# Kernel tuning notes

Measured on AMD Instinct MI355X. Metric: run time of the kernel, lower is better.

Reference implementation:

```python
import jax, jax.numpy as jnp
import numpy as np

C = 256
GROUPS = 8
EPS_GN = 1e-5
EPS_ATTN = 1e-6


def setup_inputs() -> dict:
    key = jax.random.key(0)
    ks = jax.random.split(key, 10)
    b, c, h, w = 8, C, 128, 128
    # xavier_uniform for 1x1 conv weight [out, in]: limit = sqrt(6/(in+out))
    lim = float(np.sqrt(6.0 / (c + c)))
    mkw = lambda k: jax.random.uniform(k, (c, c), jnp.float32, -lim, lim)
    return {
        "x": jax.random.normal(ks[0], (b, c, h, w), jnp.float32),
        "gamma": jnp.ones((c,), jnp.float32),
        "beta": jnp.zeros((c,), jnp.float32),
        "Wq": mkw(ks[1]), "bq": jnp.zeros((c,), jnp.float32),
        "Wk": mkw(ks[2]), "bk": jnp.zeros((c,), jnp.float32),
        "Wv": mkw(ks[3]), "bv": jnp.zeros((c,), jnp.float32),
        "Wp": mkw(ks[4]), "bp": jnp.zeros((c,), jnp.float32),
    }


def _group_norm(x, gamma, beta):
    b, c, h, w = x.shape
    xg = x.reshape(b, GROUPS, c // GROUPS, h, w)
    mean = xg.mean(axis=(2, 3, 4), keepdims=True)
    var = xg.var(axis=(2, 3, 4), keepdims=True)
    xn = ((xg - mean) * jax.lax.rsqrt(var + EPS_GN)).reshape(b, c, h, w)
    return xn * gamma[None, :, None, None] + beta[None, :, None, None]


def _conv1x1(x, W, bias):
    # 1x1 conv == per-pixel matmul: [b,c,h,w] x [o,c] -> [b,o,h,w]
    return jnp.einsum('bchw,oc->bohw', x, W) + bias[None, :, None, None]


def reference(x, gamma, beta, Wq, bq, Wk, bk, Wv, bv, Wp, bp):
    b, c, h, w = x.shape
    xn = _group_norm(x, gamma, beta)
    q = jax.nn.elu(_conv1x1(xn, Wq, bq)) + 1.0
    k = jax.nn.elu(_conv1x1(xn, Wk, bk)) + 1.0
    v = _conv1x1(xn, Wv, bv)
    n = h * w
    q = q.reshape(b, c, n)
    k = k.reshape(b, c, n)
    v = v.reshape(b, c, n)
    kv = jnp.einsum('bcn,bdn->bcd', k, v)          # k @ v^T, [b,c,c]
    k_sum = jnp.sum(k, axis=2, keepdims=True)       # [b,c,1]
    kv = kv / (k_sum + EPS_ATTN)
    out = jnp.einsum('bcd,bdn->bcn', kv, q).reshape(b, c, h, w)
    out = _conv1x1(out, Wp, bp)
    return out + x
```

## Files before the change

kernel.cpp:

```cpp
#include <hip/hip_runtime.h>

typedef unsigned short u16;
using bf16x8 = __attribute__((ext_vector_type(8))) __bf16;
using f32x4  = __attribute__((ext_vector_type(4))) float;

#define BATCH 8
#define CH    256
#define NPIX  16384
#define GN_EPS   1e-5f
#define ATTN_EPS 1e-6f

__device__ __forceinline__ u16 f2bf(float f) {
  unsigned int u = __float_as_uint(f);
  u += 0x7fffu + ((u >> 16) & 1u);
  return (u16)(u >> 16);
}

__global__ void stats_kernel(const float* __restrict__ x, float* __restrict__ sum,
                             float* __restrict__ sqs) {
  const int gi = blockIdx.x >> 3;
  const int sp = blockIdx.x & 7;
  const float4* p = (const float4*)x + (size_t)gi * 131072 + (size_t)sp * 16384;
  float s = 0.f, ss = 0.f;
  for (int i = 0; i < 64; ++i) {
    float4 v = p[threadIdx.x + i * 256];
    s  += v.x + v.y + v.z + v.w;
    ss += v.x * v.x + v.y * v.y + v.z * v.z + v.w * v.w;
  }
  for (int off = 32; off; off >>= 1) {
    s  += __shfl_xor(s, off);
    ss += __shfl_xor(ss, off);
  }
  __shared__ float rs[4], rss[4];
  const int wave = threadIdx.x >> 6, lane = threadIdx.x & 63;
  if (!lane) { rs[wave] = s; rss[wave] = ss; }
  __syncthreads();
  if (!threadIdx.x) {
    atomicAdd(&sum[gi], rs[0] + rs[1] + rs[2] + rs[3]);
    atomicAdd(&sqs[gi], rss[0] + rss[1] + rss[2] + rss[3]);
  }
}

__global__ void finalize_kernel(const float* __restrict__ sums, const float* __restrict__ sqs,
                                const float* __restrict__ gamma, const float* __restrict__ beta,
                                float* __restrict__ sA, float* __restrict__ sB) {
  const int t = blockIdx.x * 256 + threadIdx.x;
  const int c = t & 255;
  const int gi = (t >> 8) * 8 + (c >> 5);
  const float inv = 1.f / 524288.f;
  const float mean = sums[gi] * inv;
  const float var = sqs[gi] * inv - mean * mean;
  const float rstd = rsqrtf(var + GN_EPS);
  const float a = rstd * gamma[c];
  sA[t] = a;
  sB[t] = beta[c] - mean * a;
}

__global__ __launch_bounds__(256) void foldw_kernel(
    const float* __restrict__ Wq, const float* __restrict__ bq,
    const float* __restrict__ Wk, const float* __restrict__ bk,
    const float* __restrict__ sA, const float* __restrict__ sB,
    u16* __restrict__ Wqb, u16* __restrict__ Wkb,
    float* __restrict__ bqf, float* __restrict__ bkf) {
  const int b = blockIdx.x >> 4;
  const int rt = blockIdx.x & 15;
  const int tid = threadIdx.x;
  const int wave = tid >> 6, lane = tid & 63;
  const float a = sA[b * 256 + tid];
  const float s = sB[b * 256 + tid];
  __shared__ float rq[4], rk[4];
  for (int i = 0; i < 16; ++i) {
    const int row = rt * 16 + i;
    const float wq = Wq[row * 256 + tid];
    const float wk = Wk[row * 256 + tid];
    Wqb[b * 65536 + row * 256 + tid] = f2bf(wq * a);
    Wkb[b * 65536 + row * 256 + tid] = f2bf(wk * a);
    float pq = wq * s, pk = wk * s;
    for (int off = 32; off; off >>= 1) {
      pq += __shfl_xor(pq, off);
      pk += __shfl_xor(pk, off);
    }
    if (!lane) { rq[wave] = pq; rk[wave] = pk; }
    __syncthreads();
    if (!tid) {
      bqf[b * 256 + row] = bq[row] + rq[0] + rq[1] + rq[2] + rq[3];
      bkf[b * 256 + row] = bk[row] + rk[0] + rk[1] + rk[2] + rk[3];
    }
    __syncthreads();
  }
}

__global__ __launch_bounds__(256) void wvt_kernel(const float* __restrict__ Wv,
                                                  float* __restrict__ Wvt) {
  __shared__ float t[16][17];
  const int ti = blockIdx.x & 15, tj = blockIdx.x >> 4;
  const int tx = threadIdx.x & 15, ty = threadIdx.x >> 4;
  t[ty][tx] = Wv[(tj * 16 + ty) * 256 + ti * 16 + tx];
  __syncthreads();
  Wvt[(ti * 16 + ty) * 256 + tj * 16 + tx] = t[tx][ty];
}

__global__ __launch_bounds__(1024, 4) void fused_t_kernel(
    const float* __restrict__ x, const u16* __restrict__ Wkb, const float* __restrict__ bkf,
    float* __restrict__ ksum, float* __restrict__ tdst, int mode) {
  __shared__ __align__(16) u16 xnv[64 * 288];
  __shared__ __align__(16) u16 xcm[256 * 72];
  __shared__ __align__(16) u16 Kcp[256 * 72];

  const int b  = blockIdx.x & 7;
  const int sp = blockIdx.x >> 3;
  const int tid = threadIdx.x;
  const int wave = tid >> 6;
  const int lane = tid & 63;
  const int m = lane & 15;
  const int q = lane >> 4;

  const int ckg = wave >> 2;
  const int cvg = wave & 3;

  const float* xb = x + (size_t)b * CH * NPIX;
  const u16* Wkbb = Wkb + b * 65536;

  float biasv[4];
#pragma unroll
  for (int r = 0; r < 4; ++r) biasv[r] = bkf[b * 256 + wave * 16 + q * 4 + r];

  f32x4 accT[4][4];
#pragma unroll
  for (int i = 0; i < 4; ++i)
#pragma unroll
    for (int j = 0; j < 4; ++j) accT[i][j] = {0.f, 0.f, 0.f, 0.f};
  float ksum_acc = 0.f;

  const int p_ = tid & 63;
  const int cq = tid >> 6;

  for (int ch = 0; ch < 8; ++ch) {
    const int pix0 = sp * 512 + ch * 64;
    __syncthreads();
#pragma unroll
    for (int i = 0; i < 4; ++i) {
      const int c = (cq + 16 * i) * 4;
      const float v0 = __builtin_nontemporal_load(&xb[(size_t)(c + 0) * NPIX + pix0 + p_]);
      const float v1 = __builtin_nontemporal_load(&xb[(size_t)(c + 1) * NPIX + pix0 + p_]);
      const float v2 = __builtin_nontemporal_load(&xb[(size_t)(c + 2) * NPIX + pix0 + p_]);
      const float v3 = __builtin_nontemporal_load(&xb[(size_t)(c + 3) * NPIX + pix0 + p_]);
      const u16 b0 = f2bf(v0), b1 = f2bf(v1), b2 = f2bf(v2), b3 = f2bf(v3);
      const unsigned int lo = (unsigned int)b0 | ((unsigned int)b1 << 16);
      const unsigned int hi = (unsigned int)b2 | ((unsigned int)b3 << 16);
      *(uint2*)&xnv[p_ * 288 + (c ^ ((p_ & 7) << 3))] = make_uint2(lo, hi);
      xcm[(c + 0) * 72 + p_] = b0;
      xcm[(c + 1) * 72 + p_] = b1;
      xcm[(c + 2) * 72 + p_] = b2;
      xcm[(c + 3) * 72 + p_] = b3;
    }
    __syncthreads();

    f32x4 ac[4];
#pragma unroll
    for (int pt = 0; pt < 4; ++pt) ac[pt] = {0.f, 0.f, 0.f, 0.f};
#pragma unroll
    for (int ks = 0; ks < 8; ++ks) {
      const bf16x8 a = *(const bf16x8*)(Wkbb + (wave * 16 + m) * 256 + ks * 32 + q * 8);
#pragma unroll
      for (int pt = 0; pt < 4; ++pt) {
        const int prow = pt * 16 + m;
        const bf16x8 bfr =
            *(const bf16x8*)&xnv[prow * 288 + ((ks * 32 + q * 8) ^ ((prow & 7) << 3))];
        ac[pt] = __builtin_amdgcn_mfma_f32_16x16x32_bf16(a, bfr, ac[pt], 0, 0, 0);
      }
    }
#pragma unroll
    for (int r = 0; r < 4; ++r) {
      const int row = wave * 16 + q * 4 + r;
#pragma unroll
      for (int pt = 0; pt < 4; ++pt) {
        float v = ac[pt][r] + biasv[r];
        v = v > 0.f ? v + 1.f : __expf(v);
        Kcp[row * 72 + pt * 16 + m] = f2bf(v);
      }
    }
    __syncthreads();

    {
      const int krow = tid & 255;
      const int kseg = tid >> 8;
      const bf16x8 k0 = *(const bf16x8*)&Kcp[krow * 72 + kseg * 16];
      const bf16x8 k1 = *(const bf16x8*)&Kcp[krow * 72 + kseg * 16 + 8];
      float s = 0.f;
#pragma unroll
      for (int j = 0; j < 8; ++j) s += (float)k0[j] + (float)k1[j];
      ksum_acc += s;
    }

#pragma unroll
    for (int ks = 0; ks < 2; ++ks) {
      bf16x8 af[4], bfv[4];
#pragma unroll
      for (int i = 0; i < 4; ++i)
        af[i] = *(const bf16x8*)&Kcp[((4 * ckg + i) * 16 + m) * 72 + ks * 32 + q * 8];
#pragma unroll
      for (int j = 0; j < 4; ++j)
        bfv[j] = *(const bf16x8*)&xcm[((4 * cvg + j) * 16 + m) * 72 + ks * 32 + q * 8];
#pragma unroll
      for (int i = 0; i < 4; ++i)
#pragma unroll
        for (int j = 0; j < 4; ++j)
          accT[i][j] = __builtin_amdgcn_mfma_f32_16x16x32_bf16(af[i], bfv[j], accT[i][j], 0, 0, 0);
    }
  }

  atomicAdd(&ksum[b * CH + (tid & 255)], ksum_acc);
  if (mode == 0) {
    float* Tp = tdst + (size_t)blockIdx.x * 65536 + wave * 4096 + lane * 4;
#pragma unroll
    for (int i = 0; i < 4; ++i)
#pragma unroll
      for (int j = 0; j < 4; ++j)
        *(f32x4*)(Tp + (i * 4 + j) * 256) = accT[i][j];
  } else {
    float* Tb2 = tdst + (size_t)b * 65536;
#pragma unroll
    for (int i = 0; i < 4; ++i)
#pragma unroll
      for (int j = 0; j < 4; ++j)
#pragma unroll
        for (int r = 0; r < 4; ++r) {
          const int row = (4 * ckg + i) * 16 + q * 4 + r;
          const int col = (4 * cvg + j) * 16 + m;
          atomicAdd(&Tb2[row * CH + col], accT[i][j][r]);
        }
  }
}

__global__ __launch_bounds__(256) void treduce_kernel(const float* __restrict__ part,
                                                      float* __restrict__ Traw) {
  const int b = blockIdx.x >> 4;
  const int w = blockIdx.x & 15;
  __shared__ float tile[64][65];
  const size_t base = (size_t)w * 4096;
  for (int k = 0; k < 16; ++k) {
    const int o = k * 256 + threadIdx.x;
    float s = 0.f;
#pragma unroll 8
    for (int sp = 0; sp < 32; ++sp)
      s += __builtin_nontemporal_load(&part[(size_t)(sp * 8 + b) * 65536 + base + o]);
    const int lanef = (o >> 2) & 63;
    const int r = o & 3;
    const int e4 = o >> 8;
    const int i = e4 >> 2, j = e4 & 3;
    const int mm = lanef & 15, qq = lanef >> 4;
    tile[i * 16 + qq * 4 + r][j * 16 + mm] = s;
  }
  __syncthreads();
  const int ckg = w >> 2, cvg = w & 3;
  float* dst = Traw + (size_t)b * 65536 + (size_t)(ckg * 64) * 256 + cvg * 64;
  const int col = threadIdx.x & 63;
  const int r0 = threadIdx.x >> 6;
#pragma unroll
  for (int k = 0; k < 16; ++k) {
    const int lr = r0 * 16 + k;
    dst[(size_t)lr * 256 + col] = tile[lr][col];
  }
}

__global__ __launch_bounds__(256) void m1_kernel(
    const float* __restrict__ Wp, const float* __restrict__ Traw,
    const float* __restrict__ ksum, const float* __restrict__ sA,
    const float* __restrict__ sB, float* __restrict__ A1, float* __restrict__ s1) {
  __shared__ float WpLT[256 * 16];
  __shared__ float ksL[256];
  const int b = blockIdx.x >> 4;
  const int rt = blockIdx.x & 15;
  const int tid = threadIdx.x;
  const float kk = ksum[b * 256 + tid];
  ksL[tid] = kk;
  const float rs = 1.f / (kk + ATTN_EPS);
#pragma unroll
  for (int r = 0; r < 16; ++r)
    WpLT[tid * 16 + r] = Wp[(rt * 16 + r) * 256 + tid] * rs;
  __syncthreads();
  float acc[16], s1a[16];
#pragma unroll
  for (int r = 0; r < 16; ++r) { acc[r] = 0.f; s1a[r] = 0.f; }
  const float* Tb = Traw + (size_t)b * 65536;
  for (int k = 0; k < 256; ++k) {
    const float v = Tb[k * 256 + tid];
    const float kv = ksL[k];
#pragma unroll
    for (int r4 = 0; r4 < 4; ++r4) {
      const f32x4 w4 = *(const f32x4*)&WpLT[k * 16 + r4 * 4];
#pragma unroll
      for (int e = 0; e < 4; ++e) {
        acc[r4 * 4 + e] += w4[e] * v;
        s1a[r4 * 4 + e] += w4[e] * kv;
      }
    }
  }
  const float av = sA[b * 256 + tid], sv = sB[b * 256 + tid];
#pragma unroll
  for (int r = 0; r < 16; ++r)
    A1[(size_t)b * 65536 + (rt * 16 + r) * 256 + tid] = av * acc[r] + sv * s1a[r];
  if (tid == 0) {
#pragma unroll
    for (int r = 0; r < 16; ++r) s1[b * 256 + rt * 16 + r] = s1a[r];
  }
}

__global__ __launch_bounds__(256) void m2_kernel(
    const float* __restrict__ A1, const float* __restrict__ Wvt,
    const float* __restrict__ bv, const float* __restrict__ s1,
    u16* __restrict__ Mb) {
  __shared__ float ALT[256 * 16];
  const int b = blockIdx.x >> 4;
  const int rt = blockIdx.x & 15;
  const int tid = threadIdx.x;
#pragma unroll
  for (int r = 0; r < 16; ++r)
    ALT[tid * 16 + r] = A1[(size_t)b * 65536 + (rt * 16 + r) * 256 + tid];
  __syncthreads();
  float acc[16];
#pragma unroll
  for (int r = 0; r < 16; ++r) acc[r] = 0.f;
  for (int ci = 0; ci < 256; ++ci) {
    const float wv = Wvt[ci * 256 + tid];
#pragma unroll
    for (int r4 = 0; r4 < 4; ++r4) {
      const f32x4 a4 = *(const f32x4*)&ALT[ci * 16 + r4 * 4];
#pragma unroll
      for (int e = 0; e < 4; ++e) acc[r4 * 4 + e] += a4[e] * wv;
    }
  }
  const float bvd = bv[tid];
#pragma unroll
  for (int r = 0; r < 16; ++r)
    Mb[(size_t)b * 65536 + (rt * 16 + r) * 256 + tid] =
        f2bf(acc[r] + bvd * s1[b * 256 + rt * 16 + r]);
}

__global__ __launch_bounds__(256, 4) void out_kernel(
    const float* __restrict__ x, const u16* __restrict__ Wqb, const float* __restrict__ bqf,
    const u16* __restrict__ Mb, const float* __restrict__ bp, float* __restrict__ out) {
  __shared__ __align__(16) u16 buf[64 * 288];
  const int b = blockIdx.x & 7;
  const int pix0 = (blockIdx.x >> 3) * 64;
  const int tid = threadIdx.x;
  const int wave = tid >> 6;
  const int lane = tid & 63;
  const int m = lane & 15;
  const int q = lane >> 4;

  const float* xb = x + (size_t)b * CH * NPIX;
  const u16* Wqbb = Wqb + b * 65536;

  const int p_ = tid & 63;
  const int cq = tid >> 6;
#pragma unroll
  for (int i = 0; i < 16; ++i) {
    const int c = (cq + 4 * i) * 4;
    const float v0 = __builtin_nontemporal_load(&xb[(size_t)(c + 0) * NPIX + pix0 + p_]);
    const float v1 = __builtin_nontemporal_load(&xb[(size_t)(c + 1) * NPIX + pix0 + p_]);
    const float v2 = __builtin_nontemporal_load(&xb[(size_t)(c + 2) * NPIX + pix0 + p_]);
    const float v3 = __builtin_nontemporal_load(&xb[(size_t)(c + 3) * NPIX + pix0 + p_]);
    const unsigned int lo = (unsigned int)f2bf(v0) | ((unsigned int)f2bf(v1) << 16);
    const unsigned int hi = (unsigned int)f2bf(v2) | ((unsigned int)f2bf(v3) << 16);
    *(uint2*)&buf[p_ * 288 + (c ^ ((p_ & 7) << 3))] = make_uint2(lo, hi);
  }
  __syncthreads();

  f32x4 aq[4][4];
#pragma unroll
  for (int pt = 0; pt < 4; ++pt)
#pragma unroll
    for (int ct = 0; ct < 4; ++ct) aq[pt][ct] = {0.f, 0.f, 0.f, 0.f};
#pragma unroll
  for (int ks = 0; ks < 8; ++ks) {
    bf16x8 af[4];
#pragma unroll
    for (int pt = 0; pt < 4; ++pt) {
      const int prow = pt * 16 + m;
      af[pt] = *(const bf16x8*)&buf[prow * 288 + ((ks * 32 + q * 8) ^ ((prow & 7) << 3))];
    }
#pragma unroll
    for (int ct = 0; ct < 4; ++ct) {
      const bf16x8 bfr = *(const bf16x8*)(Wqbb + ((4 * wave + ct) * 16 + m) * 256 + ks * 32 + q * 8);
#pragma unroll
      for (int pt = 0; pt < 4; ++pt)
        aq[pt][ct] = __builtin_amdgcn_mfma_f32_16x16x32_bf16(af[pt], bfr, aq[pt][ct], 0, 0, 0);
    }
  }
  __syncthreads();
#pragma unroll
  for (int ct = 0; ct < 4; ++ct) {
    const int c2 = (4 * wave + ct) * 16 + m;
    const float bias = bqf[b * 256 + c2];
#pragma unroll
    for (int pt = 0; pt < 4; ++pt)
#pragma unroll
      for (int r = 0; r < 4; ++r) {
        float v = aq[pt][ct][r] + bias;
        v = v > 0.f ? v + 1.f : __expf(v);
        const int prow = pt * 16 + q * 4 + r;
        buf[prow * 288 + (c2 ^ ((prow & 7) << 3))] = f2bf(v);
      }
  }
  __syncthreads();

  f32x4 ao[4][4];
#pragma unroll
  for (int ct = 0; ct < 4; ++ct)
#pragma unroll
    for (int pt = 0; pt < 4; ++pt) ao[ct][pt] = {0.f, 0.f, 0.f, 0.f};
  const u16* Ab = Mb + (size_t)b * 65536;
#pragma unroll
  for (int ks = 0; ks < 8; ++ks) {
    bf16x8 af2[4];
#pragma unroll
    for (int ct = 0; ct < 4; ++ct)
      af2[ct] = *(const bf16x8*)(Ab + ((4 * wave + ct) * 16 + m) * 256 + ks * 32 + q * 8);
#pragma unroll
    for (int pt = 0; pt < 4; ++pt) {
      const int brow = pt * 16 + m;
      const bf16x8 bfr = *(const bf16x8*)&buf[brow * 288 + ((ks * 32 + q * 8) ^ ((brow & 7) << 3))];
#pragma unroll
      for (int ct = 0; ct < 4; ++ct)
        ao[ct][pt] = __builtin_amdgcn_mfma_f32_16x16x32_bf16(af2[ct], bfr, ao[ct][pt], 0, 0, 0);
    }
  }
  float* ob = out + (size_t)b * CH * NPIX;
#pragma unroll
  for (int ct = 0; ct < 4; ++ct)
#pragma unroll
    for (int r = 0; r < 4; ++r) {
      const int row = (4 * wave + ct) * 16 + q * 4 + r;
      const float bias = bp[row];
#pragma unroll
      for (int pt = 0; pt < 4; ++pt) {
        const int idx = row * NPIX + pix0 + pt * 16 + m;
        const float xr = __builtin_nontemporal_load(&xb[idx]);
        ob[idx] = ao[ct][pt][r] + bias + xr;
      }
    }
}

extern "C" void kernel_launch(void* const* d_in, const int* in_sizes, int n_in,
                              void* d_out, int out_size, void* d_ws, size_t ws_size,
                              hipStream_t stream) {
  const float* x     = (const float*)d_in[0];
  const float* gamma = (const float*)d_in[1];
  const float* beta  = (const float*)d_in[2];
  const float* Wq    = (const float*)d_in[3];
  const float* bq    = (const float*)d_in[4];
  const float* Wk    = (const float*)d_in[5];
  const float* bk    = (const float*)d_in[6];
  const float* Wv    = (const float*)d_in[7];
  const float* bv    = (const float*)d_in[8];
  const float* Wp    = (const float*)d_in[9];
  const float* bp    = (const float*)d_in[10];
  float* out = (float*)d_out;

  float* wsf  = (float*)d_ws;
  float* sum  = wsf;
  float* sqs  = wsf + 64;
  float* ksum = wsf + 128;
  float* sA   = wsf + 2176;
  float* sB   = wsf + 4224;
  float* s1   = wsf + 6272;
  float* bkf  = wsf + 8320;
  float* bqf  = wsf + 10368;
  float* Wvt  = wsf + 12416;
  float* Traw = wsf + 77952;
  float* A1   = wsf + 602240;
  u16* Wqb = (u16*)(wsf + 1126528);
  u16* Wkb = Wqb + 524288;
  u16* Mb  = (u16*)(wsf + 1650816);

  const bool bigws = ws_size >= ((size_t)72 << 20);
  float* Tpart = bigws ? (wsf + ((size_t)1 << 21)) : Traw;
  const int mode = bigws ? 0 : 1;

  hipMemsetAsync(wsf, 0, (size_t)(bigws ? 2176 : 602240) * sizeof(float), stream);
  stats_kernel<<<512, 256, 0, stream>>>(x, sum, sqs);
  finalize_kernel<<<8, 256, 0, stream>>>(sum, sqs, gamma, beta, sA, sB);
  wvt_kernel<<<256, 256, 0, stream>>>(Wv, Wvt);
  foldw_kernel<<<128, 256, 0, stream>>>(Wq, bq, Wk, bk, sA, sB, Wqb, Wkb, bqf, bkf);
  fused_t_kernel<<<256, 1024, 0, stream>>>(x, Wkb, bkf, ksum, Tpart, mode);
  if (bigws) treduce_kernel<<<128, 256, 0, stream>>>(Tpart, Traw);
  m1_kernel<<<128, 256, 0, stream>>>(Wp, Traw, ksum, sA, sB, A1, s1);
  m2_kernel<<<128, 256, 0, stream>>>(A1, Wvt, bv, s1, Mb);
  out_kernel<<<2048, 256, 0, stream>>>(x, Wqb, bqf, Mb, bp, out);
}
```

Baseline: 616.5 us.

## Prefetch next x chunk into registers, hoist Wk fragments, merge transpose into finalize

Within fused_t_kernel, the x loads for the next 64-pixel chunk are issued into registers right after the current chunk is written to LDS, so global-load latency overlaps with the MFMA work. The Wk bf16 fragments are loaded once into registers before the loop instead of on every chunk. The Wv transpose kernel is folded into finalize_kernel as extra blocks to save one launch. The cost is higher register pressure (16 prefetched floats plus 8 bf16x8 fragments) in a 1024-thread block bounded to 4 waves per SIMD, which could cause spills.

Result: slower. 659.7 us (+7.0%).

```diff
diff --git a/kernel.cpp b/kernel.cpp
--- a/kernel.cpp
+++ b/kernel.cpp
@@ -43,17 +43,28 @@
 
 __global__ void finalize_kernel(const float* __restrict__ sums, const float* __restrict__ sqs,
                                 const float* __restrict__ gamma, const float* __restrict__ beta,
-                                float* __restrict__ sA, float* __restrict__ sB) {
-  const int t = blockIdx.x * 256 + threadIdx.x;
-  const int c = t & 255;
-  const int gi = (t >> 8) * 8 + (c >> 5);
-  const float inv = 1.f / 524288.f;
-  const float mean = sums[gi] * inv;
-  const float var = sqs[gi] * inv - mean * mean;
-  const float rstd = rsqrtf(var + GN_EPS);
-  const float a = rstd * gamma[c];
-  sA[t] = a;
-  sB[t] = beta[c] - mean * a;
+                                float* __restrict__ sA, float* __restrict__ sB,
+                                const float* __restrict__ Wv, float* __restrict__ Wvt) {
+  if (blockIdx.x < 8) {
+    const int t = blockIdx.x * 256 + threadIdx.x;
+    const int c = t & 255;
+    const int gi = (t >> 8) * 8 + (c >> 5);
+    const float inv = 1.f / 524288.f;
+    const float mean = sums[gi] * inv;
+    const float var = sqs[gi] * inv - mean * mean;
+    const float rstd = rsqrtf(var + GN_EPS);
+    const float a = rstd * gamma[c];
+    sA[t] = a;
+    sB[t] = beta[c] - mean * a;
+  } else {
+    __shared__ float t[16][17];
+    const int bid = blockIdx.x - 8;
+    const int ti = bid & 15, tj = bid >> 4;
+    const int tx = threadIdx.x & 15, ty = threadIdx.x >> 4;
+    t[ty][tx] = Wv[(tj * 16 + ty) * 256 + ti * 16 + tx];
+    __syncthreads();
+    Wvt[(ti * 16 + ty) * 256 + tj * 16 + tx] = t[tx][ty];
+  }
 }
 
 __global__ __launch_bounds__(256) void foldw_kernel(
@@ -90,16 +101,6 @@
   }
 }
 
-__global__ __launch_bounds__(256) void wvt_kernel(const float* __restrict__ Wv,
-                                                  float* __restrict__ Wvt) {
-  __shared__ float t[16][17];
-  const int ti = blockIdx.x & 15, tj = blockIdx.x >> 4;
-  const int tx = threadIdx.x & 15, ty = threadIdx.x >> 4;
-  t[ty][tx] = Wv[(tj * 16 + ty) * 256 + ti * 16 + tx];
-  __syncthreads();
-  Wvt[(ti * 16 + ty) * 256 + tj * 16 + tx] = t[tx][ty];
-}
-
 __global__ __launch_bounds__(1024, 4) void fused_t_kernel(
     const float* __restrict__ x, const u16* __restrict__ Wkb, const float* __restrict__ bkf,
     float* __restrict__ ksum, float* __restrict__ tdst, int mode) {
@@ -121,6 +122,11 @@
   const float* xb = x + (size_t)b * CH * NPIX;
   const u16* Wkbb = Wkb + b * 65536;
 
+  bf16x8 wA[8];
+#pragma unroll
+  for (int ks = 0; ks < 8; ++ks)
+    wA[ks] = *(const bf16x8*)(Wkbb + (wave * 16 + m) * 256 + ks * 32 + q * 8);
+
   float biasv[4];
 #pragma unroll
   for (int r = 0; r < 4; ++r) biasv[r] = bkf[b * 256 + wave * 16 + q * 4 + r];
@@ -135,17 +141,24 @@
   const int p_ = tid & 63;
   const int cq = tid >> 6;
 
-  for (int ch = 0; ch < 8; ++ch) {
-    const int pix0 = sp * 512 + ch * 64;
-    __syncthreads();
+  float v[4][4];
+  {
+    const int pix0 = sp * 512;
 #pragma unroll
     for (int i = 0; i < 4; ++i) {
       const int c = (cq + 16 * i) * 4;
-      const float v0 = __builtin_nontemporal_load(&xb[(size_t)(c + 0) * NPIX + pix0 + p_]);
-      const float v1 = __builtin_nontemporal_load(&xb[(size_t)(c + 1) * NPIX + pix0 + p_]);
-      const float v2 = __builtin_nontemporal_load(&xb[(size_t)(c + 2) * NPIX + pix0 + p_]);
-      const float v3 = __builtin_nontemporal_load(&xb[(size_t)(c + 3) * NPIX + pix0 + p_]);
-      const u16 b0 = f2bf(v0), b1 = f2bf(v1), b2 = f2bf(v2), b3 = f2bf(v3);
+#pragma unroll
+      for (int j = 0; j < 4; ++j)
+        v[i][j] = __builtin_nontemporal_load(&xb[(size_t)(c + j) * NPIX + pix0 + p_]);
+    }
+  }
+
+  for (int ch = 0; ch < 8; ++ch) {
+    __syncthreads();
+#pragma unroll
+    for (int i = 0; i < 4; ++i) {
+      const int c = (cq + 16 * i) * 4;
+      const u16 b0 = f2bf(v[i][0]), b1 = f2bf(v[i][1]), b2 = f2bf(v[i][2]), b3 = f2bf(v[i][3]);
       const unsigned int lo = (unsigned int)b0 | ((unsigned int)b1 << 16);
       const unsigned int hi = (unsigned int)b2 | ((unsigned int)b3 << 16);
       *(uint2*)&xnv[p_ * 288 + (c ^ ((p_ & 7) << 3))] = make_uint2(lo, hi);
@@ -154,6 +167,16 @@
       xcm[(c + 2) * 72 + p_] = b2;
       xcm[(c + 3) * 72 + p_] = b3;
     }
+    if (ch < 7) {
+      const int pix0n = sp * 512 + (ch + 1) * 64;
+#pragma unroll
+      for (int i = 0; i < 4; ++i) {
+        const int c = (cq + 16 * i) * 4;
+#pragma unroll
+        for (int j = 0; j < 4; ++j)
+          v[i][j] = __builtin_nontemporal_load(&xb[(size_t)(c + j) * NPIX + pix0n + p_]);
+      }
+    }
     __syncthreads();
 
     f32x4 ac[4];
@@ -161,13 +184,12 @@
     for (int pt = 0; pt < 4; ++pt) ac[pt] = {0.f, 0.f, 0.f, 0.f};
 #pragma unroll
     for (int ks = 0; ks < 8; ++ks) {
-      const bf16x8 a = *(const bf16x8*)(Wkbb + (wave * 16 + m) * 256 + ks * 32 + q * 8);
 #pragma unroll
       for (int pt = 0; pt < 4; ++pt) {
         const int prow = pt * 16 + m;
         const bf16x8 bfr =
             *(const bf16x8*)&xnv[prow * 288 + ((ks * 32 + q * 8) ^ ((prow & 7) << 3))];
-        ac[pt] = __builtin_amdgcn_mfma_f32_16x16x32_bf16(a, bfr, ac[pt], 0, 0, 0);
+        ac[pt] = __builtin_amdgcn_mfma_f32_16x16x32_bf16(wA[ks], bfr, ac[pt], 0, 0, 0);
       }
     }
 #pragma unroll
@@ -175,9 +197,9 @@
       const int row = wave * 16 + q * 4 + r;
 #pragma unroll
       for (int pt = 0; pt < 4; ++pt) {
-        float v = ac[pt][r] + biasv[r];
-        v = v > 0.f ? v + 1.f : __expf(v);
-        Kcp[row * 72 + pt * 16 + m] = f2bf(v);
+        float vv = ac[pt][r] + biasv[r];
+        vv = vv > 0.f ? vv + 1.f : __expf(vv);
+        Kcp[row * 72 + pt * 16 + m] = f2bf(vv);
       }
     }
     __syncthreads();
@@ -481,8 +503,7 @@
 
   hipMemsetAsync(wsf, 0, (size_t)(bigws ? 2176 : 602240) * sizeof(float), stream);
   stats_kernel<<<512, 256, 0, stream>>>(x, sum, sqs);
-  finalize_kernel<<<8, 256, 0, stream>>>(sum, sqs, gamma, beta, sA, sB);
-  wvt_kernel<<<256, 256, 0, stream>>>(Wv, Wvt);
+  finalize_kernel<<<264, 256, 0, stream>>>(sum, sqs, gamma, beta, sA, sB, Wv, Wvt);
   foldw_kernel<<<128, 256, 0, stream>>>(Wq, bq, Wk, bk, sA, sB, Wqb, Wkb, bqf, bkf);
   fused_t_kernel<<<256, 1024, 0, stream>>>(x, Wkb, bkf, ksum, Tpart, mode);
   if (bigws) treduce_kernel<<<128, 256, 0, stream>>>(Tpart, Traw);
```
